# Kernel tuning notes

Measured on AMD Instinct MI355X. Metric: run time of the kernel, lower is better.

Reference implementation:

```python
import jax, jax.numpy as jnp
import numpy as np

B, L, D, K = 8, 256, 256, 64  # batch, slots, n_input, attn_dimension


def setup_inputs() -> dict:
    key = jax.random.key(0)
    k1, k2, k3 = jax.random.split(key, 3)
    inputs = jax.random.normal(k1, (B, L, D), dtype=jnp.float32)
    # torch.nn.Linear weights are [out_features, in_features]; scale to avoid tanh saturation
    W1 = jax.random.normal(k2, (K, 2 * D), dtype=jnp.float32) * (1.0 / np.sqrt(2 * D))
    W2 = jax.random.normal(k3, (1, K), dtype=jnp.float32) * (1.0 / np.sqrt(K))
    return {"inputs": inputs, "W1": W1, "W2": W2}


def reference(inputs, W1, W2):
    # CONCAT branch of SlotAttention:
    #   score[b,i,j] = W2 @ tanh(W1 @ concat(inputs[b,i], inputs[b,j]))
    # Split W1 into the halves acting on the i-part and j-part of the concat
    # (identical math, avoids materializing the [B,L,L,2D] concat tensor).
    d = inputs.shape[-1]
    W1i, W1j = W1[:, :d], W1[:, d:]
    qi = jnp.einsum('bld,kd->blk', inputs, W1i)          # [B,L,K]
    kj = jnp.einsum('bld,kd->blk', inputs, W1j)          # [B,L,K]
    h = jnp.tanh(qi[:, :, None, :] + kj[:, None, :, :])  # [B,L,L,K]
    scores = jnp.einsum('bijk,k->bij', h, W2[0])         # [B,L,L]
    attn = jax.nn.softmax(scores, axis=2)                # softmax over j
    context = jnp.einsum('bij,bjd->bid', attn, inputs)   # [B,L,D]
    return jnp.concatenate([inputs, context], axis=2)    # [B,L,2D]
```

## Files before the change

kernel.cpp:

```cpp
#include <hip/hip_runtime.h>


#define Bn 8
#define Ln 256
#define Dn 256
#define Kn 64
#define ROWS (Bn*Ln)
#define IPB 2

__global__ __launch_bounds__(256) void proj_kernel(
    const float* __restrict__ X,
    const float* __restrict__ W1,
    float* __restrict__ QK)
{
    __shared__ float Xs[4 * Dn];
    __shared__ float pr[128 * 4];
    const int tid = threadIdx.x;
    const int r0 = blockIdx.x * 4;

    ((float4*)Xs)[tid] = ((const float4*)(X + r0 * Dn))[tid];
    __syncthreads();

    const int c    = tid & 127;
    const int dh   = tid >> 7;
    const int k    = c & 63;
    const int half = c >> 6;
    const float4* Wrow = (const float4*)(W1 + k * (2 * Dn) + half * Dn + dh * (Dn / 2));
    const float4* x0p = (const float4*)(Xs + 0 * Dn + dh * (Dn / 2));
    const float4* x1p = (const float4*)(Xs + 1 * Dn + dh * (Dn / 2));
    const float4* x2p = (const float4*)(Xs + 2 * Dn + dh * (Dn / 2));
    const float4* x3p = (const float4*)(Xs + 3 * Dn + dh * (Dn / 2));
    float a0 = 0.f, a1 = 0.f, a2 = 0.f, a3 = 0.f;
    #pragma unroll 8
    for (int d4 = 0; d4 < 32; ++d4) {
        float4 w  = Wrow[d4];
        float4 x0 = x0p[d4], x1 = x1p[d4], x2 = x2p[d4], x3 = x3p[d4];
        a0 = fmaf(w.x, x0.x, a0); a0 = fmaf(w.y, x0.y, a0);
        a0 = fmaf(w.z, x0.z, a0); a0 = fmaf(w.w, x0.w, a0);
        a1 = fmaf(w.x, x1.x, a1); a1 = fmaf(w.y, x1.y, a1);
        a1 = fmaf(w.z, x1.z, a1); a1 = fmaf(w.w, x1.w, a1);
        a2 = fmaf(w.x, x2.x, a2); a2 = fmaf(w.y, x2.y, a2);
        a2 = fmaf(w.z, x2.z, a2); a2 = fmaf(w.w, x2.w, a2);
        a3 = fmaf(w.x, x3.x, a3); a3 = fmaf(w.y, x3.y, a3);
        a3 = fmaf(w.z, x3.z, a3); a3 = fmaf(w.w, x3.w, a3);
    }
    if (dh) ((float4*)pr)[c] = make_float4(a0, a1, a2, a3);
    __syncthreads();
    if (!dh) {
        float4 p = ((const float4*)pr)[c];
        QK[(r0 + 0) * 128 + c] = __expf(2.0f * (a0 + p.x));
        QK[(r0 + 1) * 128 + c] = __expf(2.0f * (a1 + p.y));
        QK[(r0 + 2) * 128 + c] = __expf(2.0f * (a2 + p.z));
        QK[(r0 + 3) * 128 + c] = __expf(2.0f * (a3 + p.w));
    }
}

__global__ __launch_bounds__(256) void attn_kernel(
    const float* __restrict__ X,
    const float* __restrict__ QK,
    const float* __restrict__ W2,
    float* __restrict__ out)
{
    __shared__ float eq_s[IPB * Kn];
    __shared__ float w2_s[Kn];
    __shared__ float S[Ln * IPB];
    __shared__ float4 red[4 * IPB * 64];

    const int tid = threadIdx.x;
    const int b  = blockIdx.x >> 7;
    const int i0 = (blockIdx.x & 127) * IPB;

    if (tid < Kn) w2_s[tid] = W2[tid];
    if (tid < IPB * Kn) {
        int ii = tid >> 6, kk = tid & 63;
        eq_s[ii * Kn + kk] = QK[(b * Ln + i0 + ii) * 128 + kk];
    }

    float ekr[Kn];
    const float4* kj4 = (const float4*)(QK + (b * Ln + tid) * 128 + 64);
    #pragma unroll
    for (int q = 0; q < 16; ++q) {
        float4 v = kj4[q];
        ekr[q * 4 + 0] = v.x; ekr[q * 4 + 1] = v.y;
        ekr[q * 4 + 2] = v.z; ekr[q * 4 + 3] = v.w;
    }
    __syncthreads();

    float s0 = 0.f, s1 = 0.f;
    {
        const float4* w4  = (const float4*)w2_s;
        const float4* q4a = (const float4*)(eq_s);
        const float4* q4b = (const float4*)(eq_s + Kn);
        #pragma unroll
        for (int k4 = 0; k4 < 16; ++k4) {
            float4 w  = w4[k4];
            float4 q0 = q4a[k4], q1 = q4b[k4];
            #pragma unroll
            for (int c = 0; c < 4; ++c) {
                float ek = ekr[k4 * 4 + c];
                float wk = (c == 0) ? w.x : (c == 1) ? w.y : (c == 2) ? w.z : w.w;
                float e0 = (c == 0) ? q0.x : (c == 1) ? q0.y : (c == 2) ? q0.z : q0.w;
                float e1 = (c == 0) ? q1.x : (c == 1) ? q1.y : (c == 2) ? q1.z : q1.w;
                s0 = fmaf(wk, __builtin_amdgcn_rcpf(fmaf(e0, ek, 1.0f)), s0);
                s1 = fmaf(wk, __builtin_amdgcn_rcpf(fmaf(e1, ek, 1.0f)), s1);
            }
        }
    }
    ((float2*)S)[tid] = make_float2(s0, s1);
    __syncthreads();

    {
        const int wv = tid >> 6, lane = tid & 63;
        if (wv < IPB) {
            float e0 = __expf(-2.0f * S[(lane      ) * IPB + wv]);
            float e1 = __expf(-2.0f * S[(lane +  64) * IPB + wv]);
            float e2 = __expf(-2.0f * S[(lane + 128) * IPB + wv]);
            float e3 = __expf(-2.0f * S[(lane + 192) * IPB + wv]);
            float sum = (e0 + e1) + (e2 + e3);
            #pragma unroll
            for (int off = 32; off > 0; off >>= 1)
                sum += __shfl_xor(sum, off);
            float inv = 1.0f / sum;
            S[(lane      ) * IPB + wv] = e0 * inv;
            S[(lane +  64) * IPB + wv] = e1 * inv;
            S[(lane + 128) * IPB + wv] = e2 * inv;
            S[(lane + 192) * IPB + wv] = e3 * inv;
        }
    }
    __syncthreads();

    {
        const int wv = tid >> 6, lane = tid & 63;
        float4 acc0 = {0,0,0,0}, acc1 = {0,0,0,0};
        const float4* Xb4 = (const float4*)(X + b * Ln * Dn);
        const float2* S2  = (const float2*)S;
        const int jbase = wv * 64;
        #pragma unroll 8
        for (int jj = 0; jj < 64; ++jj) {
            int j = jbase + jj;
            float2 at = S2[j];
            float4 x  = Xb4[j * 64 + lane];
            acc0.x = fmaf(at.x, x.x, acc0.x); acc0.y = fmaf(at.x, x.y, acc0.y);
            acc0.z = fmaf(at.x, x.z, acc0.z); acc0.w = fmaf(at.x, x.w, acc0.w);
            acc1.x = fmaf(at.y, x.x, acc1.x); acc1.y = fmaf(at.y, x.y, acc1.y);
            acc1.z = fmaf(at.y, x.z, acc1.z); acc1.w = fmaf(at.y, x.w, acc1.w);
        }
        red[(wv * IPB + 0) * 64 + lane] = acc0;
        red[(wv * IPB + 1) * 64 + lane] = acc1;
    }
    __syncthreads();

    {
        const int i = (tid & 127) >> 6, q = tid & 63;
        const int row = b * Ln + i0 + i;
        if (tid < 128) {
            float4 p0 = red[(0 * IPB + i) * 64 + q];
            float4 p1 = red[(1 * IPB + i) * 64 + q];
            float4 p2 = red[(2 * IPB + i) * 64 + q];
            float4 p3 = red[(3 * IPB + i) * 64 + q];
            float4 c;
            c.x = (p0.x + p1.x) + (p2.x + p3.x);
            c.y = (p0.y + p1.y) + (p2.y + p3.y);
            c.z = (p0.z + p1.z) + (p2.z + p3.z);
            c.w = (p0.w + p1.w) + (p2.w + p3.w);
            ((float4*)(out + row * 2 * Dn + Dn))[q] = c;
        } else {
            float4 xcopy = ((const float4*)(X + row * Dn))[q];
            ((float4*)(out + row * 2 * Dn))[q] = xcopy;
        }
    }
}

extern "C" void kernel_launch(void* const* d_in, const int* in_sizes, int n_in,
                              void* d_out, int out_size, void* d_ws, size_t ws_size,
                              hipStream_t stream) {
    const float* X  = (const float*)d_in[0];
    const float* W1 = (const float*)d_in[1];
    const float* W2 = (const float*)d_in[2];
    float* out = (float*)d_out;
    float* QK  = (float*)d_ws;

    proj_kernel<<<ROWS / 4, 256, 0, stream>>>(X, W1, QK);
    attn_kernel<<<ROWS / IPB, 256, 0, stream>>>(X, QK, W2, out);
}
```

Before: 84.96 us.

## Process four query rows per block with 512 threads splitting K dimension

The attention kernel now handles four query rows per block instead of two and uses 512 threads. Each j column is split across two threads that each cover half of the K dimension, and the partial scores are summed in shared memory before the softmax. The context pass reads each X row once for four outputs, which halves the X reuse traffic per output row, and the block count is halved. In exchange shared memory and the reduction get larger, and the per-thread key register array is halved, which should help occupancy.

New measurement: 79.15 us (median of 2 runs). -6.8%, faster.

```diff
diff --git a/kernel.cpp b/kernel.cpp
--- a/kernel.cpp
+++ b/kernel.cpp
@@ -6,7 +6,7 @@
 #define Dn 256
 #define Kn 64
 #define ROWS (Bn*Ln)
-#define IPB 2
+#define IPB 4
 
 __global__ __launch_bounds__(256) void proj_kernel(
     const float* __restrict__ X,
@@ -55,7 +55,7 @@
     }
 }
 
-__global__ __launch_bounds__(256) void attn_kernel(
+__global__ __launch_bounds__(512, 4) void attn_kernel(
     const float* __restrict__ X,
     const float* __restrict__ QK,
     const float* __restrict__ W2,
@@ -63,111 +63,134 @@
 {
     __shared__ float eq_s[IPB * Kn];
     __shared__ float w2_s[Kn];
-    __shared__ float S[Ln * IPB];
-    __shared__ float4 red[4 * IPB * 64];
+    __shared__ float Sp[2 * IPB * Ln];
+    __shared__ float4 S4[Ln];
+    __shared__ float4 red[8 * IPB * 64];
 
     const int tid = threadIdx.x;
-    const int b  = blockIdx.x >> 7;
-    const int i0 = (blockIdx.x & 127) * IPB;
+    const int b  = blockIdx.x >> 6;
+    const int i0 = (blockIdx.x & 63) * IPB;
+    const int j  = tid & 255;
+    const int kh = tid >> 8;
 
     if (tid < Kn) w2_s[tid] = W2[tid];
-    if (tid < IPB * Kn) {
-        int ii = tid >> 6, kk = tid & 63;
+    if (tid >= 256) {
+        int t = tid - 256;
+        int ii = t >> 6, kk = t & 63;
         eq_s[ii * Kn + kk] = QK[(b * Ln + i0 + ii) * 128 + kk];
     }
 
-    float ekr[Kn];
-    const float4* kj4 = (const float4*)(QK + (b * Ln + tid) * 128 + 64);
-    #pragma unroll
-    for (int q = 0; q < 16; ++q) {
-        float4 v = kj4[q];
-        ekr[q * 4 + 0] = v.x; ekr[q * 4 + 1] = v.y;
-        ekr[q * 4 + 2] = v.z; ekr[q * 4 + 3] = v.w;
-    }
-    __syncthreads();
-
-    float s0 = 0.f, s1 = 0.f;
-    {
-        const float4* w4  = (const float4*)w2_s;
-        const float4* q4a = (const float4*)(eq_s);
-        const float4* q4b = (const float4*)(eq_s + Kn);
+    float ekr[32];
+    {
+        const float4* kj4 = (const float4*)(QK + (b * Ln + j) * 128 + 64 + kh * 32);
         #pragma unroll
-        for (int k4 = 0; k4 < 16; ++k4) {
+        for (int q = 0; q < 8; ++q) {
+            float4 v = kj4[q];
+            ekr[q * 4 + 0] = v.x; ekr[q * 4 + 1] = v.y;
+            ekr[q * 4 + 2] = v.z; ekr[q * 4 + 3] = v.w;
+        }
+    }
+    __syncthreads();
+
+    {
+        float s0 = 0.f, s1 = 0.f, s2 = 0.f, s3 = 0.f;
+        const float4* w4  = ((const float4*)w2_s) + kh * 8;
+        const float4* q4a = ((const float4*)(eq_s          )) + kh * 8;
+        const float4* q4b = ((const float4*)(eq_s +     Kn )) + kh * 8;
+        const float4* q4c = ((const float4*)(eq_s + 2 * Kn )) + kh * 8;
+        const float4* q4d = ((const float4*)(eq_s + 3 * Kn )) + kh * 8;
+        #pragma unroll
+        for (int k4 = 0; k4 < 8; ++k4) {
             float4 w  = w4[k4];
-            float4 q0 = q4a[k4], q1 = q4b[k4];
+            float4 q0 = q4a[k4], q1 = q4b[k4], q2 = q4c[k4], q3 = q4d[k4];
             #pragma unroll
             for (int c = 0; c < 4; ++c) {
                 float ek = ekr[k4 * 4 + c];
                 float wk = (c == 0) ? w.x : (c == 1) ? w.y : (c == 2) ? w.z : w.w;
                 float e0 = (c == 0) ? q0.x : (c == 1) ? q0.y : (c == 2) ? q0.z : q0.w;
                 float e1 = (c == 0) ? q1.x : (c == 1) ? q1.y : (c == 2) ? q1.z : q1.w;
+                float e2 = (c == 0) ? q2.x : (c == 1) ? q2.y : (c == 2) ? q2.z : q2.w;
+                float e3 = (c == 0) ? q3.x : (c == 1) ? q3.y : (c == 2) ? q3.z : q3.w;
                 s0 = fmaf(wk, __builtin_amdgcn_rcpf(fmaf(e0, ek, 1.0f)), s0);
                 s1 = fmaf(wk, __builtin_amdgcn_rcpf(fmaf(e1, ek, 1.0f)), s1);
+                s2 = fmaf(wk, __builtin_amdgcn_rcpf(fmaf(e2, ek, 1.0f)), s2);
+                s3 = fmaf(wk, __builtin_amdgcn_rcpf(fmaf(e3, ek, 1.0f)), s3);
             }
         }
-    }
-    ((float2*)S)[tid] = make_float2(s0, s1);
+        Sp[(kh * IPB + 0) * Ln + j] = s0;
+        Sp[(kh * IPB + 1) * Ln + j] = s1;
+        Sp[(kh * IPB + 2) * Ln + j] = s2;
+        Sp[(kh * IPB + 3) * Ln + j] = s3;
+    }
     __syncthreads();
 
     {
         const int wv = tid >> 6, lane = tid & 63;
         if (wv < IPB) {
-            float e0 = __expf(-2.0f * S[(lane      ) * IPB + wv]);
-            float e1 = __expf(-2.0f * S[(lane +  64) * IPB + wv]);
-            float e2 = __expf(-2.0f * S[(lane + 128) * IPB + wv]);
-            float e3 = __expf(-2.0f * S[(lane + 192) * IPB + wv]);
+            const float* p0 = Sp + wv * Ln;
+            const float* p1 = Sp + (IPB + wv) * Ln;
+            float T0 = p0[lane      ] + p1[lane      ];
+            float T1 = p0[lane +  64] + p1[lane +  64];
+            float T2 = p0[lane + 128] + p1[lane + 128];
+            float T3 = p0[lane + 192] + p1[lane + 192];
+            float e0 = __expf(-2.0f * T0);
+            float e1 = __expf(-2.0f * T1);
+            float e2 = __expf(-2.0f * T2);
+            float e3 = __expf(-2.0f * T3);
             float sum = (e0 + e1) + (e2 + e3);
             #pragma unroll
             for (int off = 32; off > 0; off >>= 1)
                 sum += __shfl_xor(sum, off);
             float inv = 1.0f / sum;
-            S[(lane      ) * IPB + wv] = e0 * inv;
-            S[(lane +  64) * IPB + wv] = e1 * inv;
-            S[(lane + 128) * IPB + wv] = e2 * inv;
-            S[(lane + 192) * IPB + wv] = e3 * inv;
+            ((float*)S4)[(lane      ) * 4 + wv] = e0 * inv;
+            ((float*)S4)[(lane +  64) * 4 + wv] = e1 * inv;
+            ((float*)S4)[(lane + 128) * 4 + wv] = e2 * inv;
+            ((float*)S4)[(lane + 192) * 4 + wv] = e3 * inv;
+        } else {
+            int t = tid - 256;
+            int ii = t >> 6, q = t & 63;
+            const int row = b * Ln + i0 + ii;
+            ((float4*)(out + row * 2 * Dn))[q] = ((const float4*)(X + row * Dn))[q];
         }
     }
     __syncthreads();
 
     {
         const int wv = tid >> 6, lane = tid & 63;
-        float4 acc0 = {0,0,0,0}, acc1 = {0,0,0,0};
+        float4 acc0 = {0,0,0,0}, acc1 = {0,0,0,0}, acc2 = {0,0,0,0}, acc3 = {0,0,0,0};
         const float4* Xb4 = (const float4*)(X + b * Ln * Dn);
-        const float2* S2  = (const float2*)S;
-        const int jbase = wv * 64;
+        const int jbase = wv * 32;
         #pragma unroll 8
-        for (int jj = 0; jj < 64; ++jj) {
-            int j = jbase + jj;
-            float2 at = S2[j];
-            float4 x  = Xb4[j * 64 + lane];
+        for (int jj = 0; jj < 32; ++jj) {
+            int jr = jbase + jj;
+            float4 at = S4[jr];
+            float4 x  = Xb4[jr * 64 + lane];
             acc0.x = fmaf(at.x, x.x, acc0.x); acc0.y = fmaf(at.x, x.y, acc0.y);
             acc0.z = fmaf(at.x, x.z, acc0.z); acc0.w = fmaf(at.x, x.w, acc0.w);
             acc1.x = fmaf(at.y, x.x, acc1.x); acc1.y = fmaf(at.y, x.y, acc1.y);
             acc1.z = fmaf(at.y, x.z, acc1.z); acc1.w = fmaf(at.y, x.w, acc1.w);
+            acc2.x = fmaf(at.z, x.x, acc2.x); acc2.y = fmaf(at.z, x.y, acc2.y);
+            acc2.z = fmaf(at.z, x.z, acc2.z); acc2.w = fmaf(at.z, x.w, acc2.w);
+            acc3.x = fmaf(at.w, x.x, acc3.x); acc3.y = fmaf(at.w, x.y, acc3.y);
+            acc3.z = fmaf(at.w, x.z, acc3.z); acc3.w = fmaf(at.w, x.w, acc3.w);
         }
         red[(wv * IPB + 0) * 64 + lane] = acc0;
         red[(wv * IPB + 1) * 64 + lane] = acc1;
-    }
-    __syncthreads();
-
-    {
-        const int i = (tid & 127) >> 6, q = tid & 63;
+        red[(wv * IPB + 2) * 64 + lane] = acc2;
+        red[(wv * IPB + 3) * 64 + lane] = acc3;
+    }
+    __syncthreads();
+
+    if (tid < 256) {
+        const int i = tid >> 6, q = tid & 63;
+        float4 c = {0, 0, 0, 0};
+        #pragma unroll
+        for (int w = 0; w < 8; ++w) {
+            float4 p = red[(w * IPB + i) * 64 + q];
+            c.x += p.x; c.y += p.y; c.z += p.z; c.w += p.w;
+        }
         const int row = b * Ln + i0 + i;
-        if (tid < 128) {
-            float4 p0 = red[(0 * IPB + i) * 64 + q];
-            float4 p1 = red[(1 * IPB + i) * 64 + q];
-            float4 p2 = red[(2 * IPB + i) * 64 + q];
-            float4 p3 = red[(3 * IPB + i) * 64 + q];
-            float4 c;
-            c.x = (p0.x + p1.x) + (p2.x + p3.x);
-            c.y = (p0.y + p1.y) + (p2.y + p3.y);
-            c.z = (p0.z + p1.z) + (p2.z + p3.z);
-            c.w = (p0.w + p1.w) + (p2.w + p3.w);
-            ((float4*)(out + row * 2 * Dn + Dn))[q] = c;
-        } else {
-            float4 xcopy = ((const float4*)(X + row * Dn))[q];
-            ((float4*)(out + row * 2 * Dn))[q] = xcopy;
-        }
+        ((float4*)(out + row * 2 * Dn + Dn))[q] = c;
     }
 }
 
@@ -181,5 +204,5 @@
     float* QK  = (float*)d_ws;
 
     proj_kernel<<<ROWS / 4, 256, 0, stream>>>(X, W1, QK);
-    attn_kernel<<<ROWS / IPB, 256, 0, stream>>>(X, QK, W2, out);
+    attn_kernel<<<ROWS / IPB, 512, 0, stream>>>(X, QK, W2, out);
 }
```
